# Kernel tuning notes

Hardware: AMD Instinct MI355X
Metric: run time of the kernel (lower is better)

The kernel has to match this reference:

```python
import jax, jax.numpy as jnp
import numpy as np

B, D, H, E = 1024, 64, 128, 8192


def setup_inputs() -> dict:
    key = jax.random.key(0)
    ks = jax.random.split(key, 10)
    def w(k, shape, fan_in):
        return jax.random.normal(k, shape, jnp.float32) / np.float32(np.sqrt(fan_in))
    return {
        "mu": jax.random.normal(ks[0], (B, D), jnp.float32),
        "current_edge_index": jax.random.randint(ks[1], (2, E), 0, B),
        "W1": w(ks[2], (D, H), D),   "b1": jnp.zeros((H,), jnp.float32),
        "W2": w(ks[3], (H, H), H),   "b2": jnp.zeros((H,), jnp.float32),
        "Ws1": w(ks[4], (2 * H, H), 2 * H), "bs1": jnp.zeros((H,), jnp.float32),
        "Ws2": w(ks[5], (H, 1), H),  "bs2": jnp.zeros((1,), jnp.float32),
        "Wg1": w(ks[6], (2 * H, H), 2 * H), "bg1": jnp.zeros((H,), jnp.float32),
        "Wg2": w(ks[7], (H, D), H), "bg2": jnp.zeros((D,), jnp.float32),
    }


def _gcn(x, W, b, src, dst, n):
    loop = jnp.arange(n)
    s = jnp.concatenate([src, loop])
    d = jnp.concatenate([dst, loop])
    deg = jax.ops.segment_sum(jnp.ones_like(s, x.dtype), d, num_segments=n)
    dinv = jax.lax.rsqrt(jnp.maximum(deg, 1e-12))
    norm = dinv[s] * dinv[d]                      # [E+n]
    xw = x @ W                                    # [n,H]
    out = jax.ops.segment_sum(xw[s] * norm[:, None], d, num_segments=n)
    return out + b


def _pairwise_scores(h, Ws1, bs1, Ws2, bs2):
    # score_mlp([h_i || h_j]) for all pairs, vectorized: split first-layer weight
    A = h @ Ws1[:H]                               # [B,H] contribution of h_i
    C = h @ Ws1[H:]                               # [B,H] contribution of h_j
    pre = jax.nn.relu(A[:, None, :] + C[None, :, :] + bs1)   # [B,B,H]
    s = (pre @ Ws2)[..., 0] + bs2[0]              # [B,B]
    up = jnp.triu(s, 1)                           # only i<j computed in original
    return up + up.T                              # symmetric, zero diagonal


def _kruskal(scores_np, n):
    iu, ju = np.triu_indices(n, 1)
    w = scores_np[iu, ju]
    order = np.argsort(-w, kind="stable")         # descending, stable like list.sort
    parent = list(range(n))
    rank = [0] * n
    def find(u):
        while parent[u] != u:
            parent[u] = parent[parent[u]]
            u = parent[u]
        return u
    edges = []
    for k in order:
        i, j = int(iu[k]), int(ju[k])
        ri, rj = find(i), find(j)
        if ri == rj:
            continue
        if rank[ri] < rank[rj]:
            parent[ri] = rj
        elif rank[ri] > rank[rj]:
            parent[rj] = ri
        else:
            parent[rj] = ri
            rank[ri] += 1
        edges.append((i, j))
        if len(edges) == n - 1:
            break
    return np.asarray(edges, dtype=np.int64)      # [n-1, 2]


def reference(mu, current_edge_index, W1, b1, W2, b2, Ws1, bs1, Ws2, bs2, Wg1, bg1, Wg2, bg2):
    src, dst = current_edge_index[0], current_edge_index[1]
    h = jax.nn.relu(_gcn(mu, W1, b1, src, dst, B))
    h = jax.nn.relu(_gcn(h, W2, b2, src, dst, B))
    scores = _pairwise_scores(h, Ws1, bs1, Ws2, bs2)          # [B,B]
    mst = _kruskal(np.asarray(scores), B)                     # [B-1,2], i<j
    ei = jnp.asarray(mst[:, 0])
    ej = jnp.asarray(mst[:, 1])
    # bidirectional edge index: src=[i,j,...], dst=[j,i,...]
    new_edge_index = jnp.stack([
        jnp.stack([ei, ej], axis=1).reshape(-1),
        jnp.stack([ej, ei], axis=1).reshape(-1),
    ], axis=0)                                                # [2, 2*(B-1)]
    hp = jnp.concatenate([h[ei], h[ej]], axis=1)              # [B-1, 2H]
    gamma = jnp.tanh(jax.nn.relu(hp @ Wg1 + bg1) @ Wg2 + bg2) # [B-1, D]
    return (new_edge_index, gamma)
```

## Files before the change

kernel.cpp:

```cpp
#include <hip/hip_runtime.h>
#include <hip/hip_bf16.h>
#include <math.h>

#define BN 1024
#define DIN 64
#define HD 128
#define EN 8192
#define SLOTS_STRIDE 64

__global__ void k_init(int* cnt, int* comp, unsigned long long* best, int* mstcnt) {
    int i = blockIdx.x * blockDim.x + threadIdx.x;
    if (i < BN) { cnt[i] = 0; comp[i] = i; best[i] = 0ull; }
    if (i == 0) *mstcnt = 0;
}

__global__ void k_fill(const int* dst, int* cnt, int* slots) {
    int e = blockIdx.x * blockDim.x + threadIdx.x;
    if (e < EN) {
        int d = dst[e];
        int p = atomicAdd(&cnt[d], 1);
        if (p < SLOTS_STRIDE) slots[d * SLOTS_STRIDE + p] = e;
    }
}

__global__ __launch_bounds__(128) void k_finish(int* slots, const int* cnt, float* dinv) {
    __shared__ int buf[128][65];
    int tid = threadIdx.x;
    int t = blockIdx.x * 128 + tid;
    int n = cnt[t];
    if (n > SLOTS_STRIDE) n = SLOTS_STRIDE;
    for (int k = 0; k < n; k++) buf[tid][k] = slots[t * SLOTS_STRIDE + k];
    for (int k = 1; k < n; k++) {
        int v = buf[tid][k];
        int q = k - 1;
        while (q >= 0 && buf[tid][q] > v) { buf[tid][q + 1] = buf[tid][q]; q--; }
        buf[tid][q + 1] = v;
    }
    for (int k = 0; k < n; k++) slots[t * SLOTS_STRIDE + k] = buf[tid][k];
    dinv[t] = 1.0f / sqrtf(fmaxf((float)(n + 1), 1e-12f));
}

__global__ __launch_bounds__(128) void k_mm(const float* x, const float* W, const float* bias,
                                            float* out, int K) {
    __shared__ float xr[HD];
    int row = blockIdx.x, col = threadIdx.x;
    if (col < K) xr[col] = x[row * K + col];
    __syncthreads();
    float acc = bias ? bias[col] : 0.0f;
    for (int k = 0; k < K; k++) acc = fmaf(xr[k], W[k * HD + col], acc);
    out[row * HD + col] = acc;
}

__global__ __launch_bounds__(128) void k_gather(const float* xw, const float* bvec, const int* src,
                                                const int* slots, const int* cnt,
                                                const float* dinv, float* hout) {
    int d = blockIdx.x, t = threadIdx.x;
    float dd = dinv[d];
    float acc = 0.0f;
    int base = d * SLOTS_STRIDE, n = cnt[d];
    if (n > SLOTS_STRIDE) n = SLOTS_STRIDE;
    for (int s = 0; s < n; s++) {
        int e = slots[base + s];
        int sn = src[e];
        acc = fmaf(xw[sn * HD + t], dinv[sn] * dd, acc);
    }
    acc = fmaf(xw[d * HD + t], dd * dd, acc);
    acc += bvec[t];
    hout[d * HD + t] = fmaxf(acc, 0.0f);
}

__global__ __launch_bounds__(256) void k_scores(const float* Aa, const float* Cc,
                                                const float* Ws2, const float* bs2v, float* S) {
    int bi = blockIdx.y, bj = blockIdx.x;
    if (bi > bj) return;
    __shared__ float As[64][68];
    __shared__ float Cs[64][68];
    __shared__ float w2[HD];
    int tid = threadIdx.x;
    int R = bi * 64, Cb = bj * 64;
    if (tid < HD) w2[tid] = Ws2[tid];
    int tx = tid & 15, ty = tid >> 4;
    float acc[4][4] = {};
    for (int half = 0; half < 2; half++) {
        int k0 = half * 64;
        __syncthreads();
        for (int idx = tid; idx < 64 * 64; idx += 256) {
            int row = idx >> 6;
            int kk = idx & 63;
            As[kk][row] = Aa[(R + row) * HD + k0 + kk];
            Cs[kk][row] = Cc[(Cb + row) * HD + k0 + kk];
        }
        __syncthreads();
        for (int kk = 0; kk < 64; kk++) {
            float4 av = *(const float4*)&As[kk][ty * 4];
            float4 cv = *(const float4*)&Cs[kk][tx * 4];
            float wk = w2[k0 + kk];
            float ar[4] = {av.x, av.y, av.z, av.w};
            float cr[4] = {cv.x, cv.y, cv.z, cv.w};
#pragma unroll
            for (int r = 0; r < 4; r++)
#pragma unroll
                for (int q = 0; q < 4; q++) {
                    float tv = fmaxf(ar[r] + cr[q], 0.0f);
                    acc[r][q] = fmaf(tv, wk, acc[r][q]);
                }
        }
    }
    float b2 = bs2v[0];
#pragma unroll
    for (int r = 0; r < 4; r++)
#pragma unroll
        for (int q = 0; q < 4; q++) {
            int gr = R + ty * 4 + r, gc = Cb + tx * 4 + q;
            float v = acc[r][q] + b2;
            if (gr < gc) { S[gr * BN + gc] = v; S[gc * BN + gr] = v; }
            else if (gr == gc) S[gr * BN + gc] = 0.0f;
        }
}

__device__ __forceinline__ unsigned long long edge_key(float w, int i, int j) {
    unsigned u = __float_as_uint(w);
    u = (u & 0x80000000u) ? ~u : (u | 0x80000000u);
    int a = i < j ? i : j, b = i < j ? j : i;
    unsigned packed = (unsigned)(a * BN + b);
    return ((unsigned long long)u << 20) | (unsigned long long)(0xFFFFFu - packed);
}

__global__ __launch_bounds__(256) void k_best(const float* S, const int* comp,
                                              unsigned long long* best) {
    int i = blockIdx.x;
    int ci = comp[i];
    unsigned long long loc = 0ull;
    for (int j = threadIdx.x; j < BN; j += 256) {
        if (comp[j] != ci) {
            unsigned long long key = edge_key(S[i * BN + j], i, j);
            if (key > loc) loc = key;
        }
    }
    __shared__ unsigned long long red[256];
    red[threadIdx.x] = loc;
    __syncthreads();
    for (int s = 128; s > 0; s >>= 1) {
        if (threadIdx.x < s) {
            unsigned long long o = red[threadIdx.x + s];
            if (o > red[threadIdx.x]) red[threadIdx.x] = o;
        }
        __syncthreads();
    }
    if (threadIdx.x == 0 && red[0]) atomicMax(&best[ci], red[0]);
}

__global__ __launch_bounds__(1024) void k_merge(int* comp, unsigned long long* best,
                                                unsigned long long* mst, int* mstcnt) {
    __shared__ int pa[BN], pb[BN];
    int c = threadIdx.x;
    int myComp = comp[c];
    bool root = (myComp == c);
    unsigned long long e = best[c];
    int t = c;
    if (root && e) {
        unsigned packed = 0xFFFFFu - (unsigned)(e & 0xFFFFFu);
        int a = packed >> 10, b = packed & 1023;
        int ca = comp[a], cb = comp[b];
        t = (ca == c) ? cb : ca;
    }
    pa[c] = (root && e) ? t : c;
    __syncthreads();
    bool mutual = root && e && (pa[t] == c);
    int p0 = pa[c];
    if (mutual && c < t) p0 = c;
    __syncthreads();
    pa[c] = p0;
    __syncthreads();
    if (root && e && !(mutual && c > t)) {
        int idx = atomicAdd(mstcnt, 1);
        mst[idx] = e;
    }
    for (int it = 0; it < 10; it++) {
        pb[c] = pa[pa[c]];
        __syncthreads();
        pa[c] = pb[c];
        __syncthreads();
    }
    comp[c] = pa[myComp];
    best[c] = 0ull;
}

__global__ __launch_bounds__(1024) void k_sort(const unsigned long long* mst, float* out, int* pairs) {
    __shared__ unsigned long long s[BN];
    int tid = threadIdx.x;
    s[tid] = (tid < BN - 1) ? mst[tid] : 0ull;
    __syncthreads();
    for (int k = 2; k <= BN; k <<= 1)
        for (int j = k >> 1; j > 0; j >>= 1) {
            int l = tid ^ j;
            if (l > tid) {
                unsigned long long x = s[tid], y = s[l];
                bool up = ((tid & k) == 0);
                if ((x > y) == up) { s[tid] = y; s[l] = x; }
            }
            __syncthreads();
        }
    if (tid < BN - 1) {
        unsigned long long key = s[BN - 1 - tid];
        unsigned packed = 0xFFFFFu - (unsigned)(key & 0xFFFFFu);
        int i = packed >> 10, j2 = packed & 1023;
        out[2 * tid] = (float)i;
        out[2 * tid + 1] = (float)j2;
        out[2046 + 2 * tid] = (float)j2;
        out[2046 + 2 * tid + 1] = (float)i;
        pairs[2 * tid] = i;
        pairs[2 * tid + 1] = j2;
    }
}

__global__ __launch_bounds__(128) void k_gamma(const float* h, const int* pairs,
                                               const float* Wg1, const float* bg1,
                                               const float* Wg2, const float* bg2, float* out) {
    int eidx = blockIdx.x;
    __shared__ float hp[2 * HD];
    __shared__ float z1[HD];
    int t = threadIdx.x;
    int i = pairs[2 * eidx], j = pairs[2 * eidx + 1];
    hp[t] = h[i * HD + t];
    hp[HD + t] = h[j * HD + t];
    __syncthreads();
    float acc = bg1[t];
    for (int k = 0; k < 2 * HD; k++) acc = fmaf(hp[k], Wg1[k * HD + t], acc);
    z1[t] = fmaxf(acc, 0.0f);
    __syncthreads();
    if (t < DIN) {
        float g = bg2[t];
        for (int k = 0; k < HD; k++) g = fmaf(z1[k], Wg2[k * DIN + t], g);
        out[4092 + eidx * DIN + t] = tanhf(g);
    }
}

extern "C" void kernel_launch(void* const* d_in, const int* in_sizes, int n_in,
                              void* d_out, int out_size, void* d_ws, size_t ws_size,
                              hipStream_t stream) {
    const float* mu  = (const float*)d_in[0];
    const int*   ei  = (const int*)d_in[1];
    const float* W1  = (const float*)d_in[2];
    const float* b1  = (const float*)d_in[3];
    const float* W2  = (const float*)d_in[4];
    const float* b2  = (const float*)d_in[5];
    const float* Ws1 = (const float*)d_in[6];
    const float* bs1 = (const float*)d_in[7];
    const float* Ws2 = (const float*)d_in[8];
    const float* bs2 = (const float*)d_in[9];
    const float* Wg1 = (const float*)d_in[10];
    const float* bg1 = (const float*)d_in[11];
    const float* Wg2 = (const float*)d_in[12];
    const float* bg2 = (const float*)d_in[13];
    float* out = (float*)d_out;

    const int* src = ei;
    const int* dst = ei + EN;

    char* ws = (char*)d_ws;
    int*   slots = (int*)(ws);
    int*   cnt   = (int*)(ws + 262144);
    float* dinv  = (float*)(ws + 266240);
    float* S     = (float*)(ws);
    float* xw    = (float*)(ws + 4194304);
    float* h1    = (float*)(ws + 4718592);
    float* h2    = (float*)(ws + 5242880);
    float* Aa    = (float*)(ws + 5767168);
    float* Cc    = (float*)(ws + 6291456);
    int*   comp  = (int*)(ws + 6815744);
    unsigned long long* best = (unsigned long long*)(ws + 6819840);
    unsigned long long* mst  = (unsigned long long*)(ws + 6828032);
    int*   mstcnt = (int*)(ws + 6836224);
    int*   pairs  = (int*)(ws + 6840320);

    k_init<<<4, 256, 0, stream>>>(cnt, comp, best, mstcnt);
    k_fill<<<EN / 256, 256, 0, stream>>>(dst, cnt, slots);
    k_finish<<<BN / 128, 128, 0, stream>>>(slots, cnt, dinv);

    k_mm<<<BN, HD, 0, stream>>>(mu, W1, nullptr, xw, DIN);
    k_gather<<<BN, HD, 0, stream>>>(xw, b1, src, slots, cnt, dinv, h1);
    k_mm<<<BN, HD, 0, stream>>>(h1, W2, nullptr, xw, HD);
    k_gather<<<BN, HD, 0, stream>>>(xw, b2, src, slots, cnt, dinv, h2);

    k_mm<<<BN, HD, 0, stream>>>(h2, Ws1, nullptr, Aa, HD);
    k_mm<<<BN, HD, 0, stream>>>(h2, Ws1 + HD * HD, bs1, Cc, HD);

    k_scores<<<dim3(16, 16), 256, 0, stream>>>(Aa, Cc, Ws2, bs2, S);

    for (int r = 0; r < 10; r++) {
        k_best<<<BN, 256, 0, stream>>>(S, comp, best);
        k_merge<<<1, 1024, 0, stream>>>(comp, best, mst, mstcnt);
    }

    k_sort<<<1, 1024, 0, stream>>>(mst, out, pairs);
    k_gamma<<<BN - 1, HD, 0, stream>>>(h2, pairs, Wg1, bg1, Wg2, bg2, out);
}
```

Measured before the change: 179.7 us.

## Fuse Boruvka best/merge into last-block kernel and batch small matmuls

Merges each Boruvka round's best-edge search and component merge into a single kernel. The last block to finish, detected with an atomic counter and threadfence, performs the merge, and later rounds exit early once the MST is complete. This removes ten single-block kernel launches and their serialization gaps. The row-per-block matmul is also replaced with an 8-rows-per-block version that reuses each weight load, and the two score projections are fused into one kernel. The risks are the extra atomics and fences and relying on the completion counter for correctness.

```diff
diff --git a/kernel.cpp b/kernel.cpp
--- a/kernel.cpp
+++ b/kernel.cpp
@@ -7,10 +7,12 @@
 #define HD 128
 #define EN 8192
 #define SLOTS_STRIDE 64
-
-__global__ void k_init(int* cnt, int* comp, unsigned long long* best, int* mstcnt) {
+#define MMR 8
+
+__global__ void k_init(int* cnt, int* comp, unsigned long long* best, int* mstcnt, int* done_ctr) {
     int i = blockIdx.x * blockDim.x + threadIdx.x;
     if (i < BN) { cnt[i] = 0; comp[i] = i; best[i] = 0ull; }
+    if (i < 16) done_ctr[i] = 0;
     if (i == 0) *mstcnt = 0;
 }
 
@@ -40,15 +42,56 @@
     dinv[t] = 1.0f / sqrtf(fmaxf((float)(n + 1), 1e-12f));
 }
 
-__global__ __launch_bounds__(128) void k_mm(const float* x, const float* W, const float* bias,
-                                            float* out, int K) {
-    __shared__ float xr[HD];
-    int row = blockIdx.x, col = threadIdx.x;
-    if (col < K) xr[col] = x[row * K + col];
-    __syncthreads();
-    float acc = bias ? bias[col] : 0.0f;
-    for (int k = 0; k < K; k++) acc = fmaf(xr[k], W[k * HD + col], acc);
-    out[row * HD + col] = acc;
+__global__ __launch_bounds__(128) void k_mm8(const float* x, const float* W, const float* bias,
+                                             float* out, int K) {
+    __shared__ float xr[MMR][HD];
+    int col = threadIdx.x;
+    int r0 = blockIdx.x * MMR;
+#pragma unroll
+    for (int r = 0; r < MMR; r++)
+        if (col < K) xr[r][col] = x[(r0 + r) * K + col];
+    __syncthreads();
+    float b = bias ? bias[col] : 0.0f;
+    float acc[MMR];
+#pragma unroll
+    for (int r = 0; r < MMR; r++) acc[r] = b;
+#pragma unroll 4
+    for (int k = 0; k < K; k++) {
+        float w = W[k * HD + col];
+#pragma unroll
+        for (int r = 0; r < MMR; r++) acc[r] = fmaf(xr[r][k], w, acc[r]);
+    }
+#pragma unroll
+    for (int r = 0; r < MMR; r++) out[(r0 + r) * HD + col] = acc[r];
+}
+
+__global__ __launch_bounds__(128) void k_mmAC(const float* h, const float* Ws1, const float* bs1,
+                                              float* Aa, float* Cc) {
+    __shared__ float xr[MMR][HD];
+    int col = threadIdx.x;
+    int r0 = blockIdx.x * MMR;
+#pragma unroll
+    for (int r = 0; r < MMR; r++) xr[r][col] = h[(r0 + r) * HD + col];
+    __syncthreads();
+    float accA[MMR], accC[MMR];
+    float bc = bs1[col];
+#pragma unroll
+    for (int r = 0; r < MMR; r++) { accA[r] = 0.0f; accC[r] = bc; }
+#pragma unroll 2
+    for (int k = 0; k < HD; k++) {
+        float wa = Ws1[k * HD + col];
+        float wc = Ws1[(HD + k) * HD + col];
+#pragma unroll
+        for (int r = 0; r < MMR; r++) {
+            accA[r] = fmaf(xr[r][k], wa, accA[r]);
+            accC[r] = fmaf(xr[r][k], wc, accC[r]);
+        }
+    }
+#pragma unroll
+    for (int r = 0; r < MMR; r++) {
+        Aa[(r0 + r) * HD + col] = accA[r];
+        Cc[(r0 + r) * HD + col] = accC[r];
+    }
 }
 
 __global__ __launch_bounds__(128) void k_gather(const float* xw, const float* bvec, const int* src,
@@ -126,64 +169,85 @@
     return ((unsigned long long)u << 20) | (unsigned long long)(0xFFFFFu - packed);
 }
 
-__global__ __launch_bounds__(256) void k_best(const float* S, const int* comp,
-                                              unsigned long long* best) {
+__global__ __launch_bounds__(256) void k_round(const float* S, int* comp,
+                                               unsigned long long* best,
+                                               unsigned long long* mst, int* mstcnt,
+                                               int* done_ctr, int round) {
+    __shared__ unsigned long long red[256];
+    __shared__ int pa[BN], pb[BN];
+    __shared__ int isLast;
+    int tid = threadIdx.x;
+    if (*mstcnt >= BN - 1) return;
     int i = blockIdx.x;
     int ci = comp[i];
     unsigned long long loc = 0ull;
-    for (int j = threadIdx.x; j < BN; j += 256) {
+    for (int j = tid; j < BN; j += 256) {
         if (comp[j] != ci) {
             unsigned long long key = edge_key(S[i * BN + j], i, j);
             if (key > loc) loc = key;
         }
     }
-    __shared__ unsigned long long red[256];
-    red[threadIdx.x] = loc;
+    red[tid] = loc;
     __syncthreads();
     for (int s = 128; s > 0; s >>= 1) {
-        if (threadIdx.x < s) {
-            unsigned long long o = red[threadIdx.x + s];
-            if (o > red[threadIdx.x]) red[threadIdx.x] = o;
-        }
-        __syncthreads();
-    }
-    if (threadIdx.x == 0 && red[0]) atomicMax(&best[ci], red[0]);
-}
-
-__global__ __launch_bounds__(1024) void k_merge(int* comp, unsigned long long* best,
-                                                unsigned long long* mst, int* mstcnt) {
-    __shared__ int pa[BN], pb[BN];
-    int c = threadIdx.x;
-    int myComp = comp[c];
-    bool root = (myComp == c);
-    unsigned long long e = best[c];
-    int t = c;
-    if (root && e) {
-        unsigned packed = 0xFFFFFu - (unsigned)(e & 0xFFFFFu);
-        int a = packed >> 10, b = packed & 1023;
-        int ca = comp[a], cb = comp[b];
-        t = (ca == c) ? cb : ca;
-    }
-    pa[c] = (root && e) ? t : c;
-    __syncthreads();
-    bool mutual = root && e && (pa[t] == c);
-    int p0 = pa[c];
-    if (mutual && c < t) p0 = c;
-    __syncthreads();
-    pa[c] = p0;
-    __syncthreads();
-    if (root && e && !(mutual && c > t)) {
-        int idx = atomicAdd(mstcnt, 1);
-        mst[idx] = e;
-    }
+        if (tid < s) {
+            unsigned long long o = red[tid + s];
+            if (o > red[tid]) red[tid] = o;
+        }
+        __syncthreads();
+    }
+    if (tid == 0) {
+        if (red[0]) atomicMax(&best[ci], red[0]);
+        __threadfence();
+        int v = atomicAdd(&done_ctr[round], 1);
+        isLast = (v == BN - 1) ? 1 : 0;
+    }
+    __syncthreads();
+    if (!isLast) return;
+    __threadfence();
+    for (int c = tid; c < BN; c += 256) {
+        int myComp = comp[c];
+        bool root = (myComp == c);
+        unsigned long long e = best[c];
+        int t = c;
+        if (root && e) {
+            unsigned packed = 0xFFFFFu - (unsigned)(e & 0xFFFFFu);
+            int a = packed >> 10, b = packed & 1023;
+            int ca = comp[a], cb = comp[b];
+            t = (ca == c) ? cb : ca;
+        }
+        pa[c] = (root && e) ? t : c;
+    }
+    __syncthreads();
+    for (int c = tid; c < BN; c += 256) {
+        int myComp = comp[c];
+        bool root = (myComp == c);
+        unsigned long long e = best[c];
+        int p0 = pa[c];
+        if (root && e) {
+            int t = pa[c];
+            bool mutual = (pa[t] == c);
+            if (mutual && c < t) p0 = c;
+            if (!(mutual && c > t)) {
+                int idx = atomicAdd(mstcnt, 1);
+                mst[idx] = e;
+            }
+        }
+        pb[c] = p0;
+    }
+    __syncthreads();
+    for (int c = tid; c < BN; c += 256) pa[c] = pb[c];
+    __syncthreads();
     for (int it = 0; it < 10; it++) {
-        pb[c] = pa[pa[c]];
-        __syncthreads();
-        pa[c] = pb[c];
-        __syncthreads();
-    }
-    comp[c] = pa[myComp];
-    best[c] = 0ull;
+        for (int c = tid; c < BN; c += 256) pb[c] = pa[pa[c]];
+        __syncthreads();
+        for (int c = tid; c < BN; c += 256) pa[c] = pb[c];
+        __syncthreads();
+    }
+    for (int c = tid; c < BN; c += 256) {
+        comp[c] = pa[comp[c]];
+        best[c] = 0ull;
+    }
 }
 
 __global__ __launch_bounds__(1024) void k_sort(const unsigned long long* mst, float* out, int* pairs) {
@@ -273,25 +337,23 @@
     unsigned long long* mst  = (unsigned long long*)(ws + 6828032);
     int*   mstcnt = (int*)(ws + 6836224);
     int*   pairs  = (int*)(ws + 6840320);
-
-    k_init<<<4, 256, 0, stream>>>(cnt, comp, best, mstcnt);
+    int*   done_ctr = (int*)(ws + 6848512);
+
+    k_init<<<4, 256, 0, stream>>>(cnt, comp, best, mstcnt, done_ctr);
     k_fill<<<EN / 256, 256, 0, stream>>>(dst, cnt, slots);
     k_finish<<<BN / 128, 128, 0, stream>>>(slots, cnt, dinv);
 
-    k_mm<<<BN, HD, 0, stream>>>(mu, W1, nullptr, xw, DIN);
+    k_mm8<<<BN / MMR, HD, 0, stream>>>(mu, W1, nullptr, xw, DIN);
     k_gather<<<BN, HD, 0, stream>>>(xw, b1, src, slots, cnt, dinv, h1);
-    k_mm<<<BN, HD, 0, stream>>>(h1, W2, nullptr, xw, HD);
+    k_mm8<<<BN / MMR, HD, 0, stream>>>(h1, W2, nullptr, xw, HD);
     k_gather<<<BN, HD, 0, stream>>>(xw, b2, src, slots, cnt, dinv, h2);
 
-    k_mm<<<BN, HD, 0, stream>>>(h2, Ws1, nullptr, Aa, HD);
-    k_mm<<<BN, HD, 0, stream>>>(h2, Ws1 + HD * HD, bs1, Cc, HD);
+    k_mmAC<<<BN / MMR, HD, 0, stream>>>(h2, Ws1, bs1, Aa, Cc);
 
     k_scores<<<dim3(16, 16), 256, 0, stream>>>(Aa, Cc, Ws2, bs2, S);
 
-    for (int r = 0; r < 10; r++) {
-        k_best<<<BN, 256, 0, stream>>>(S, comp, best);
-        k_merge<<<1, 1024, 0, stream>>>(comp, best, mst, mstcnt);
-    }
+    for (int r = 0; r < 10; r++)
+        k_round<<<BN, 256, 0, stream>>>(S, comp, best, mst, mstcnt, done_ctr, r);
 
     k_sort<<<1, 1024, 0, stream>>>(mst, out, pairs);
     k_gamma<<<BN - 1, HD, 0, stream>>>(h2, pairs, Wg1, bg1, Wg2, bg2, out);
```

Result: slower. 188.2 us (+4.7%).
